# Optimization experiments

Hardware: AMD Instinct MI355X
Metric: run time of the kernel (lower is better)

## Reference

```python
import jax, jax.numpy as jnp
import numpy as np

KSIZE = 3
BJORCK_ITERS = 20
POWER_ITERS = 10


def _power_iteration_sigma(A, u):
    # A: [K, n, n], u: [K, n, 1] -> leading singular value per matrix, [K]
    for _ in range(POWER_ITERS):
        v = jnp.swapaxes(A, -1, -2) @ u
        v = v / jnp.linalg.norm(v, axis=-2, keepdims=True)
        u = A @ v
        u = u / jnp.linalg.norm(u, axis=-2, keepdims=True)
    s = (jnp.swapaxes(u, -1, -2) @ A @ v)[..., 0, 0]
    return s


def _bjorck(w, u):
    # power-iteration scaling is done under no_grad in torch -> stop_gradient
    s = jax.lax.stop_gradient(_power_iteration_sigma(jax.lax.stop_gradient(w), u))
    w = w / s[:, None, None]
    for _ in range(BJORCK_ITERS):
        wtw = jnp.swapaxes(w, -1, -2) @ w
        w = 1.5 * w - 0.5 * (w @ wtw)  # beta = 0.5, first order
    return w


def _block_orth(p1, p2):
    # -> [2, 2, n, n]
    n = p1.shape[0]
    I = jnp.eye(n, dtype=p1.dtype)
    return jnp.stack([
        jnp.stack([p1 @ p2, p1 @ (I - p2)]),
        jnp.stack([(I - p1) @ p2, (I - p1) @ (I - p2)]),
    ])


def _matrix_conv(m1, m2):
    # m1: [k,k,n,n], m2: [l,l,n,n] -> [k+l-1, k+l-1, n, n]
    k, l = m1.shape[0], m2.shape[0]
    size = k + l - 1
    rows = []
    for i in range(size):
        row = []
        for j in range(size):
            acc = 0.0
            for i1 in range(min(k, i + 1)):
                for j1 in range(min(k, j + 1)):
                    if i - i1 < l and j - j1 < l:
                        acc = acc + m1[i1, j1] @ m2[i - i1, j - j1]
            row.append(acc)
        rows.append(jnp.stack(row))
    return jnp.stack(rows)


def _bcop_weight(param_matrices, init_u):
    K, C, _ = param_matrices.shape  # K = 2*(KSIZE-1)+1, C = max_channels
    ortho = _bjorck(param_matrices, init_u)
    H = ortho[0]  # cin == cout == C, full slice
    half = C // 2
    mask = jnp.concatenate(
        [jnp.ones((K - 1, 1, half), ortho.dtype), jnp.zeros((K - 1, 1, C - half), ortho.dtype)],
        axis=-1)
    PQ = ortho[1:] * mask
    PQ = PQ @ jnp.swapaxes(PQ, -1, -2)  # symmetric projections [K-1, C, C]
    p = _block_orth(PQ[0], PQ[1])
    for t in range(1, KSIZE - 1):
        p = _matrix_conv(p, _block_orth(PQ[2 * t], PQ[2 * t + 1]))
    p = jnp.einsum('ab,ijbc->ijac', H, p)  # H @ p[i,j]
    # dict_to_tensor(...).permute(3, 2, 1, 0): [k, k, r, c] -> [c, r, j, i]
    return jnp.transpose(p, (3, 2, 1, 0))  # [C_out, C_in, KSIZE, KSIZE]


def setup_inputs() -> dict:
    key = jax.random.key(0)
    k1, k2, k3, k4 = jax.random.split(key, 4)
    C = 256
    num_kernels = 2 * (KSIZE - 1) + 1
    x = jax.random.normal(k1, (32, C, 64, 64), dtype=jnp.float32)
    param_matrices = jax.random.normal(k2, (num_kernels, C, C), dtype=jnp.float32) / np.sqrt(C)
    init_u = jax.random.normal(k3, (num_kernels, C, 1), dtype=jnp.float32)
    bias = jax.random.uniform(k4, (C,), dtype=jnp.float32, minval=-1.0 / np.sqrt(C), maxval=1.0 / np.sqrt(C))
    return {"x": x, "param_matrices": param_matrices, "init_u": init_u, "bias": bias}


def reference(x, param_matrices, init_u, bias):
    weight = _bcop_weight(param_matrices, init_u)
    # cyclic (circular) padding by k//2 on each side, odd kernel
    pad = KSIZE // 2
    xp = jnp.pad(x, ((0, 0), (0, 0), (pad, pad), (pad, pad)), mode='wrap')
    out = jax.lax.conv_general_dilated(
        xp, weight, window_strides=(1, 1), padding='VALID',
        dimension_numbers=('NCHW', 'OIHW', 'NCHW'))
    return out + bias[None, :, None, None]
```

## Files before the change

kernel.cpp:

```cpp
#include <hip/hip_runtime.h>
#include <stdint.h>

typedef unsigned short u16;
typedef unsigned short u16x4 __attribute__((ext_vector_type(4)));
typedef short bf16x8 __attribute__((ext_vector_type(8)));
typedef float f32x4 __attribute__((ext_vector_type(4)));

#define CDIM 256
#define MSZ 65536

constexpr size_t O_XB   = 0;
constexpr size_t O_AT   = 67108864;
constexpr size_t O_PQH  = 67108864;
constexpr size_t O_PQL  = O_PQH + 524288;
constexpr size_t O_SVAL = 68419584;
constexpr size_t O_W0   = 68419840;
constexpr size_t O_W1   = 71041280;
constexpr size_t O_PH   = 71041280;
constexpr size_t O_PL   = O_PH + 524288;
constexpr size_t O_QTH  = O_PL + 524288;
constexpr size_t O_QTL  = O_QTH + 524288;
constexpr size_t O_TH   = 73662720;
constexpr size_t O_TL   = O_TH + 655360;
constexpr size_t O_RTH  = 74973440;
constexpr size_t O_RTL  = O_RTH + 1179648;
constexpr size_t O_WBQ  = O_RTL + 1179648;

__device__ __forceinline__ u16 f2bf(float f) {
  union { float f; uint32_t u; } a; a.f = f;
  uint32_t u = a.u;
  uint32_t r = u + 0x7FFFu + ((u >> 16) & 1u);
  return (u16)(r >> 16);
}
__device__ __forceinline__ float bf2f(u16 u) {
  union { uint32_t u; float f; } a; a.u = ((uint32_t)u) << 16; return a.f;
}
__device__ __forceinline__ void split_st(u16* hi, u16* lo, float v) {
  u16 h = f2bf(v);
  *hi = h;
  *lo = f2bf(v - bf2f(h));
}
__device__ __forceinline__ void gl16(const void* g, void* l) {
  __builtin_amdgcn_global_load_lds(
      (const __attribute__((address_space(1))) void*)g,
      (__attribute__((address_space(3))) void*)l, 16, 0, 0);
}

__device__ __forceinline__ void cvt_block(const float* __restrict__ x,
                                          u16* __restrict__ xb, int b, char* smem) {
  float (*t)[33] = (float(*)[33])smem;
  int ctile = b & 7, wtile = (b >> 3) & 1, h = (b >> 4) & 63, n = b >> 10;
  int c0 = ctile * 32, w0 = wtile * 32;
  int tid = threadIdx.x;
  #pragma unroll
  for (int p = 0; p < 4; p++) {
    int e = tid + p * 256; int cc = e >> 5, ww = e & 31;
    t[cc][ww] = x[(((size_t)n * 256 + c0 + cc) * 64 + h) * 64 + w0 + ww];
  }
  __syncthreads();
  {
    int ww = tid >> 3, c4 = (tid & 7) * 4;
    u16x4 v;
    #pragma unroll
    for (int j = 0; j < 4; ++j) v[j] = f2bf(t[c4 + j][ww]);
    *(u16x4*)&xb[(((size_t)n * 64 + h) * 64 + w0 + ww) * 256 + c0 + c4] = v;
  }
}

__global__ void wtwA_k(const float* __restrict__ W, float* __restrict__ T) {
  int m = blockIdx.y;
  int i0 = (blockIdx.x >> 3) * 32, j0 = (blockIdx.x & 7) * 32;
  const float* A = W + (size_t)m * MSZ;
  __shared__ float As[32][33], Bs[32][33];
  int tid = threadIdx.x, tx = tid & 15, ty = tid >> 4;
  float a00 = 0, a01 = 0, a10 = 0, a11 = 0;
  for (int kc = 0; kc < CDIM; kc += 32) {
    __syncthreads();
    for (int p = 0; p < 4; p++) {
      int e = tid + p * 256; int kk = e >> 5, cc = e & 31;
      As[kk][cc] = A[(kc + kk) * CDIM + i0 + cc];
      Bs[kk][cc] = A[(kc + kk) * CDIM + j0 + cc];
    }
    __syncthreads();
    #pragma unroll
    for (int kk = 0; kk < 32; kk++) {
      float av0 = As[kk][ty], av1 = As[kk][ty + 16];
      float bv0 = Bs[kk][tx], bv1 = Bs[kk][tx + 16];
      a00 += av0 * bv0; a01 += av0 * bv1; a10 += av1 * bv0; a11 += av1 * bv1;
    }
  }
  float* Tm = T + (size_t)m * MSZ;
  Tm[(i0 + ty) * CDIM + j0 + tx] = a00;
  Tm[(i0 + ty) * CDIM + j0 + tx + 16] = a01;
  Tm[(i0 + ty + 16) * CDIM + j0 + tx] = a10;
  Tm[(i0 + ty + 16) * CDIM + j0 + tx + 16] = a11;
}

__global__ __launch_bounds__(1024) void powerB_k(const float* __restrict__ A,
                                                 const float* __restrict__ B,
                                                 const float* __restrict__ u0,
                                                 float* __restrict__ sval) {
  int m = blockIdx.x;
  int tid = threadIdx.x;
  int t = tid & 255, s = tid >> 8;
  __shared__ float v[256], part[4][257];
  const float* Am = A + (size_t)m * MSZ;
  const float* Bm = B + (size_t)m * MSZ;
  float a = 0.f;
  #pragma unroll 16
  for (int i = 0; i < 64; ++i) a += Am[(s * 64 + i) * 256 + t] * u0[m * 256 + s * 64 + i];
  part[s][t] = a;
  __syncthreads();
  if (s == 0) v[t] = part[0][t] + part[1][t] + part[2][t] + part[3][t];
  __syncthreads();
  for (int it = 0; it < 9; ++it) {
    float b = 0.f;
    #pragma unroll 16
    for (int j = 0; j < 64; ++j) b += Bm[(s * 64 + j) * 256 + t] * v[s * 64 + j];
    part[s][t] = b;
    __syncthreads();
    if (s == 0) v[t] = part[0][t] + part[1][t] + part[2][t] + part[3][t];
    __syncthreads();
  }
  float b = 0.f;
  #pragma unroll 16
  for (int j = 0; j < 64; ++j) b += Bm[(s * 64 + j) * 256 + t] * v[s * 64 + j];
  part[s][t] = b;
  __syncthreads();
  if (s == 0) {
    float w = part[0][t] + part[1][t] + part[2][t] + part[3][t];
    float vv = v[t];
    float d1 = vv * w, d2 = vv * vv;
    for (int off = 32; off; off >>= 1) {
      d1 += __shfl_down(d1, off);
      d2 += __shfl_down(d2, off);
    }
    if ((t & 63) == 0) { part[1][t >> 6] = d1; part[2][t >> 6] = d2; }
  }
  __syncthreads();
  if (tid == 0) {
    float num = part[1][0] + part[1][1] + part[1][2] + part[1][3];
    float den = part[2][0] + part[2][1] + part[2][2] + part[2][3];
    sval[m] = sqrtf(num / den);
  }
}

__global__ void scaleT_k(const float* __restrict__ param, const float* __restrict__ sval,
                         u16* __restrict__ Wh, u16* __restrict__ Wl,
                         u16* __restrict__ Wth, u16* __restrict__ Wtl) {
  __shared__ float tl[32][33];
  int m = blockIdx.y;
  int i0 = (blockIdx.x >> 3) * 32, j0 = (blockIdx.x & 7) * 32;
  int tid = threadIdx.x;
  float inv = 1.0f / sval[m];
  const float* Am = param + (size_t)m * MSZ;
  size_t mo = (size_t)m * MSZ;
  for (int p = 0; p < 4; ++p) {
    int e = tid + p * 256; int ii = e >> 5, jj = e & 31;
    float v = Am[(i0 + ii) * 256 + j0 + jj] * inv;
    tl[ii][jj] = v;
    size_t idx = mo + (size_t)(i0 + ii) * 256 + j0 + jj;
    split_st(&Wh[idx], &Wl[idx], v);
  }
  __syncthreads();
  for (int p = 0; p < 4; ++p) {
    int e = tid + p * 256; int jj = e >> 5, ii = e & 31;
    float v = tl[ii][jj];
    size_t idxT = mo + (size_t)(j0 + jj) * 256 + i0 + ii;
    split_st(&Wth[idxT], &Wtl[idxT], v);
  }
}

__device__ __forceinline__ void gemm32_acc(
    const u16* __restrict__ Ah, const u16* __restrict__ Al, int i0,
    const u16* __restrict__ Bh, const u16* __restrict__ Bl, int j0,
    int K, f32x4* acc, char* smem, int tid)
{
  int lane = tid & 63, wave = tid >> 6;
  int qm = wave >> 1, qn = wave & 1;
  int ra = qm * 16 + (lane & 15);
  int rb = qn * 16 + (lane & 15);
  int kb = (lane >> 4) * 16;
  for (int kc = 0; kc < K; kc += 128) {
    __syncthreads();
    #pragma unroll
    for (int p = 0; p < 8; ++p) {
      int e = tid + p * 256;
      int bufi = e >> 9;
      int r = (e >> 4) & 31;
      int cb = (e & 15) * 16;
      const u16* srcm = (bufi == 0) ? Ah : (bufi == 1) ? Al : (bufi == 2) ? Bh : Bl;
      int r0 = (bufi < 2) ? i0 : j0;
      const char* src = (const char*)srcm + ((size_t)(r0 + r) * 256 + kc) * 2 + cb;
      *(uint4*)(smem + bufi * 8192 + r * 256 + (cb ^ ((r & 7) << 4))) = *(const uint4*)src;
    }
    __syncthreads();
    #pragma unroll
    for (int ks = 0; ks < 4; ++ks) {
      int kbyte = ks * 64 + kb;
      int oa = ra * 256 + (kbyte ^ ((ra & 7) << 4));
      int ob = rb * 256 + (kbyte ^ ((rb & 7) << 4));
      bf16x8 ah = *(const bf16x8*)(smem + oa);
      bf16x8 al = *(const bf16x8*)(smem + 8192 + oa);
      bf16x8 bh = *(const bf16x8*)(smem + 16384 + ob);
      bf16x8 bl = *(const bf16x8*)(smem + 24576 + ob);
      *acc = __builtin_amdgcn_mfma_f32_16x16x32_bf16(ah, bh, *acc, 0, 0, 0);
      *acc = __builtin_amdgcn_mfma_f32_16x16x32_bf16(ah, bl, *acc, 0, 0, 0);
      *acc = __builtin_amdgcn_mfma_f32_16x16x32_bf16(al, bh, *acc, 0, 0, 0);
    }
  }
}

#define GEMM_IDX \
  int tid = threadIdx.x; \
  int lane = tid & 63, wave = tid >> 6, qm = wave >> 1, qn = wave & 1; \
  int orow = qm * 16 + ((lane >> 4) << 2); \
  int ocol = qn * 16 + (lane & 15); \
  int i0 = (blockIdx.x >> 3) * 32, j0 = (blockIdx.x & 7) * 32; \
  __shared__ char smem[32768];

__global__ __launch_bounds__(256) void bjorck_t_k(
    const u16* __restrict__ Wth, const u16* __restrict__ Wtl,
    u16* __restrict__ Th, u16* __restrict__ Tl,
    const float* __restrict__ x, u16* __restrict__ xb, int cvt_base) {
  __shared__ char smem[32768];
  int bx = blockIdx.x;
  if (bx >= 320) {
    int b = cvt_base + bx - 320;
    if (b < 32768) cvt_block(x, xb, b, smem);
    return;
  }
  int tid = threadIdx.x;
  int lane = tid & 63, wave = tid >> 6, qm = wave >> 1, qn = wave & 1;
  int orow = qm * 16 + ((lane >> 4) << 2);
  int ocol = qn * 16 + (lane & 15);
  int i0 = ((bx & 63) >> 3) * 32, j0 = (bx & 7) * 32;
  size_t mo = (size_t)(bx >> 6) * MSZ;
  f32x4 acc = {};
  gemm32_acc(Wth + mo, Wtl + mo, i0, Wth + mo, Wtl + mo, j0, 256, &acc, smem, tid);
  #pragma unroll
  for (int v = 0; v < 4; ++v) {
    size_t idx = mo + (size_t)(i0 + orow + v) * 256 + (j0 + ocol);
    split_st(&Th[idx], &Tl[idx], acc[v]);
  }
}

__global__ __launch_bounds__(256) void bjorck_u_k(
    const u16* __restrict__ Wh, const u16* __restrict__ Wl,
    const u16* __restrict__ Th, const u16* __restrict__ Tl,
    u16* __restrict__ nWh, u16* __restrict__ nWl,
    u16* __restrict__ nWth, u16* __restrict__ nWtl,
    const float* __restrict__ x, u16* __restrict__ xb, int cvt_base) {
  __shared__ char smem[32768];
  int bx = blockIdx.x;
  if (bx >= 320) {
    int b = cvt_base + bx - 320;
    if (b < 32768) cvt_block(x, xb, b, smem);
    return;
  }
  int tid = threadIdx.x;
  int lane = tid & 63, wave = tid >> 6, qm = wave >> 1, qn = wave & 1;
  int orow = qm * 16 + ((lane >> 4) << 2);
  int ocol = qn * 16 + (lane & 15);
  int i0 = ((bx & 63) >> 3) * 32, j0 = (bx & 7) * 32;
  size_t mo = (size_t)(bx >> 6) * MSZ;
  f32x4 acc = {};
  gemm32_acc(Wh + mo, Wl + mo, i0, Th + mo, Tl + mo, j0, 256, &acc, smem, tid);
  #pragma unroll
  for (int v = 0; v < 4; ++v) {
    int r = i0 + orow + v, c = j0 + ocol;
    size_t idx = mo + (size_t)r * 256 + c;
    float wv = bf2f(Wh[idx]) + bf2f(Wl[idx]);
    float nv = 1.5f * wv - 0.5f * acc[v];
    split_st(&nWh[idx], &nWl[idx], nv);
    size_t idxT = mo + (size_t)c * 256 + r;
    split_st(&nWth[idxT], &nWtl[idxT], nv);
  }
}

__global__ __launch_bounds__(256) void pq_k(
    const u16* __restrict__ Wh, const u16* __restrict__ Wl,
    u16* __restrict__ PQh, u16* __restrict__ PQl) {
  GEMM_IDX
  int m4 = blockIdx.y;
  const u16* Oh = Wh + (size_t)(1 + m4) * MSZ;
  const u16* Ol = Wl + (size_t)(1 + m4) * MSZ;
  f32x4 acc = {};
  gemm32_acc(Oh, Ol, i0, Oh, Ol, j0, 128, &acc, smem, tid);
  #pragma unroll
  for (int v = 0; v < 4; ++v) {
    size_t idx = (size_t)m4 * MSZ + (size_t)(i0 + orow + v) * 256 + (j0 + ocol);
    split_st(&PQh[idx], &PQl[idx], acc[v]);
  }
}

__global__ __launch_bounds__(256) void c12b_k(
    const u16* __restrict__ PQh, const u16* __restrict__ PQl,
    u16* __restrict__ Ph, u16* __restrict__ Pl,
    u16* __restrict__ QTh, u16* __restrict__ QTl) {
  GEMM_IDX
  f32x4 a1 = {}, a2t = {};
  gemm32_acc(PQh, PQl, i0, PQh + MSZ, PQl + MSZ, j0, 256, &a1, smem, tid);
  gemm32_acc(PQh + 3 * MSZ, PQl + 3 * MSZ, i0, PQh + 2 * MSZ, PQl + 2 * MSZ, j0,
             256, &a2t, smem, tid);
  #pragma unroll
  for (int v = 0; v < 4; ++v) {
    int row = i0 + orow + v, col = j0 + ocol;
    size_t g = (size_t)row * 256 + col;
    float I = (row == col) ? 1.f : 0.f;
    float p0 = bf2f(PQh[g]) + bf2f(PQl[g]);
    float p1 = bf2f(PQh[MSZ + g]) + bf2f(PQl[MSZ + g]);
    float c1 = a1[v];
    split_st(&Ph[g],           &Pl[g],           c1);
    split_st(&Ph[MSZ + g],     &Pl[MSZ + g],     p0 - c1);
    split_st(&Ph[2*MSZ + g],   &Pl[2*MSZ + g],   p1 - c1);
    split_st(&Ph[3*MSZ + g],   &Pl[3*MSZ + g],   I - p0 - p1 + c1);
    float q0 = bf2f(PQh[2*MSZ + g]) + bf2f(PQl[2*MSZ + g]);
    float q1 = bf2f(PQh[3*MSZ + g]) + bf2f(PQl[3*MSZ + g]);
    float c2t = a2t[v];
    split_st(&QTh[g],          &QTl[g],          c2t);
    split_st(&QTh[MSZ + g],    &QTl[MSZ + g],    q0 - c2t);
    split_st(&QTh[2*MSZ + g],  &QTl[2*MSZ + g],  q1 - c2t);
    split_st(&QTh[3*MSZ + g],  &QTl[3*MSZ + g],  I - q0 - q1 + c2t);
  }
}

__global__ __launch_bounds__(256) void mconv_k(
    const u16* __restrict__ Ph, const u16* __restrict__ Pl,
    const u16* __restrict__ QTh, const u16* __restrict__ QTl,
    u16* __restrict__ RTh, u16* __restrict__ RTl) {
  GEMM_IDX
  int ij = blockIdx.y;
  const int toff[10] = {0, 1, 3, 4, 6, 10, 12, 13, 15, 16};
  const int tp[16] = {0, 0, 1, 1, 0, 2, 0, 1, 2, 3, 1, 3, 2, 2, 3, 3};
  const int tq[16] = {0, 1, 0, 1, 2, 0, 3, 2, 1, 0, 3, 1, 2, 3, 2, 3};
  f32x4 acc = {};
  for (int t = toff[ij]; t < toff[ij + 1]; ++t) {
    gemm32_acc(Ph + (size_t)tp[t] * MSZ, Pl + (size_t)tp[t] * MSZ, i0,
               QTh + (size_t)tq[t] * MSZ, QTl + (size_t)tq[t] * MSZ, j0, 256, &acc, smem, tid);
  }
  #pragma unroll
  for (int v = 0; v < 4; ++v) {
    int r = i0 + orow + v, c = j0 + ocol;
    size_t idxT = (size_t)ij * MSZ + (size_t)c * 256 + r;
    split_st(&RTh[idxT], &RTl[idxT], acc[v]);
  }
}

__global__ __launch_bounds__(256) void final_k(
    const u16* __restrict__ Hh, const u16* __restrict__ Hl,
    const u16* __restrict__ RTh, const u16* __restrict__ RTl,
    u16* __restrict__ WBQ) {
  GEMM_IDX
  int ij = blockIdx.y;
  f32x4 acc = {};
  gemm32_acc(Hh, Hl, i0, RTh + (size_t)ij * MSZ, RTl + (size_t)ij * MSZ, j0,
             256, &acc, smem, tid);
  #pragma unroll
  for (int v = 0; v < 4; ++v) {
    int r = i0 + orow + v, c = j0 + ocol;
    int ct = r >> 6, ks = (r >> 5) & 1, jj = (r >> 3) & 3, e = r & 7;
    int s = jj ^ ((c >> 1) & 3);
    int g = ct * 18 + ij * 2 + ks;
    WBQ[(size_t)g * 8192 + (size_t)(c * 4 + s) * 8 + e] = f2bf(acc[v]);
  }
}

__global__ __launch_bounds__(512, 2) void conv_k(
    const u16* __restrict__ xb, const u16* __restrict__ Wb,
    const float* __restrict__ bias, float* __restrict__ out) {
  int braw = blockIdx.x;
  int L = (braw & 7) * 128 + (braw >> 3);
  int h2 = L & 31, n = L >> 5;
  int h0 = h2 * 2;
  int tid = threadIdx.x;
  int lane = tid & 63, wave = tid >> 6;
  int wm = wave >> 2, wn = wave & 3;
  int fr = lane & 15, q = lane >> 4;

  __shared__ char smem[65536];
  char* sX = smem;
  char* sW = smem + 32768;

  f32x4 acc[4][4] = {};

  auto issueX = [&](int ct) {
    #pragma unroll
    for (int i = 0; i < 4; ++i) {
      int d = (wave * 4 + i) * 64 + lane;
      int cb = (d & 7) * 16;
      int w = (d >> 3) & 63;
      int r = d >> 9;
      int hs = (h0 - 1 + r) & 63;
      const char* src = (const char*)xb + (((size_t)(n * 64 + hs) * 64 + w) << 9)
                        + ct * 128 + (cb ^ ((w & 7) << 4));
      gl16(src, sX + (wave * 4 + i) * 1024);
    }
  };
  auto issueW = [&](int g) {
    const char* base = (const char*)Wb + (size_t)g * 16384;
    char* dst = sW + (g & 1) * 16384;
    #pragma unroll
    for (int i = 0; i < 2; ++i) {
      int c = (wave * 2 + i) * 64 + lane;
      gl16(base + c * 16, dst + (wave * 2 + i) * 1024);
    }
  };

  issueX(0);
  issueW(0);
  __syncthreads();

  for (int g = 0; g < 72; ++g) {
    int ct = g / 18, r18 = g % 18, tap = r18 >> 1, ks = r18 & 1;
    int kh = tap % 3, kw = tap / 3;
    if (g + 1 < 72) issueW(g + 1);
    const char* wb = sW + (g & 1) * 16384;
    __builtin_amdgcn_s_setprio(1);
    {
      bf16x8 af[4], bfr[4];
      #pragma unroll
      for (int fn = 0; fn < 4; ++fn) {
        int cl = wn * 64 + fn * 16 + fr;
        bfr[fn] = *(const bf16x8*)(wb + cl * 64 + ((q ^ ((cl >> 1) & 3)) << 4));
      }
      int kb2 = ks * 64 + q * 16;
      #pragma unroll
      for (int fm = 0; fm < 4; ++fm) {
        int wsrc = (fm * 16 + fr + kw + 63) & 63;
        af[fm] = *(const bf16x8*)(sX + ((wm + kh) * 64 + wsrc) * 128 + (kb2 ^ ((wsrc & 7) << 4)));
      }
      #pragma unroll
      for (int fm = 0; fm < 4; ++fm)
        #pragma unroll
        for (int fn = 0; fn < 4; ++fn)
          acc[fm][fn] = __builtin_amdgcn_mfma_f32_16x16x32_bf16(af[fm], bfr[fn], acc[fm][fn], 0, 0, 0);
    }
    __builtin_amdgcn_s_setprio(0);
    if (r18 == 17 && ct < 3) {
      __syncthreads();
      issueX(ct + 1);
      __syncthreads();
    } else {
      __syncthreads();
    }
  }

  __syncthreads();
  float* sF = (float*)smem;
  #pragma unroll
  for (int r = 0; r < 2; ++r) {
    if ((wn >> 1) == r) {
      #pragma unroll
      for (int fn = 0; fn < 4; ++fn) {
        int cl = (wn & 1) * 64 + fn * 16 + fr;
        float bv = bias[r * 128 + cl];
        #pragma unroll
        for (int fm = 0; fm < 4; ++fm) {
          f32x4 v = acc[fm][fn];
          v[0] += bv; v[1] += bv; v[2] += bv; v[3] += bv;
          *(f32x4*)((char*)sF + cl * 512 + wm * 256 +
                    (((unsigned)(fm * 64 + q * 16)) ^ ((unsigned)(cl & 7) << 4))) = v;
        }
      }
    }
    __syncthreads();
    #pragma unroll
    for (int p = 0; p < 8; ++p) {
      int e = tid + p * 512;
      int w4 = e & 15, hloc = (e >> 4) & 1, cl = e >> 5;
      f32x4 val = *(const f32x4*)((const char*)sF + cl * 512 + hloc * 256 +
                                  (((unsigned)(w4 * 16)) ^ ((unsigned)(cl & 7) << 4)));
      *(f32x4*)(out + (((size_t)n * 256 + r * 128 + cl) * 64 + (h0 + hloc)) * 64 + w4 * 4) = val;
    }
    if (r == 0) __syncthreads();
  }
}

extern "C" void kernel_launch(void* const* d_in, const int* in_sizes, int n_in,
                              void* d_out, int out_size, void* d_ws, size_t ws_size,
                              hipStream_t stream) {
  const float* x = (const float*)d_in[0];
  const float* param = (const float*)d_in[1];
  const float* u0 = (const float*)d_in[2];
  const float* bias = (const float*)d_in[3];
  float* out = (float*)d_out;
  char* ws = (char*)d_ws;
  (void)in_sizes; (void)n_in; (void)out_size; (void)ws_size;

  float* B = (float*)(ws + O_AT);
  float* sval = (float*)(ws + O_SVAL);
  u16* xb = (u16*)(ws + O_XB);
  u16* W0h  = (u16*)(ws + O_W0);   u16* W0l  = W0h + 327680;
  u16* W0th = W0l + 327680;        u16* W0tl = W0th + 327680;
  u16* W1h  = (u16*)(ws + O_W1);   u16* W1l  = W1h + 327680;
  u16* W1th = W1l + 327680;        u16* W1tl = W1th + 327680;
  u16* Th = (u16*)(ws + O_TH);     u16* Tl = (u16*)(ws + O_TL);
  u16* PQh = (u16*)(ws + O_PQH);   u16* PQl = (u16*)(ws + O_PQL);
  u16* Ph = (u16*)(ws + O_PH);     u16* Pl = (u16*)(ws + O_PL);
  u16* QTh = (u16*)(ws + O_QTH);   u16* QTl = (u16*)(ws + O_QTL);
  u16* RTh = (u16*)(ws + O_RTH);   u16* RTl = (u16*)(ws + O_RTL);
  u16* WBQ = (u16*)(ws + O_WBQ);

  wtwA_k<<<dim3(64, 5), 256, 0, stream>>>(param, B);
  powerB_k<<<5, 1024, 0, stream>>>(param, B, u0, sval);
  scaleT_k<<<dim3(64, 5), 256, 0, stream>>>(param, sval, W0h, W0l, W0th, W0tl);

  u16 *cWh = W0h, *cWl = W0l, *cWth = W0th, *cWtl = W0tl;
  u16 *nWh = W1h, *nWl = W1l, *nWth = W1th, *nWtl = W1tl;
  for (int it = 0; it < 20; ++it) {
    bjorck_t_k<<<1140, 256, 0, stream>>>(cWth, cWtl, Th, Tl,
                                         x, xb, (2 * it) * 820);
    bjorck_u_k<<<1140, 256, 0, stream>>>(cWh, cWl, Th, Tl, nWh, nWl, nWth, nWtl,
                                         x, xb, (2 * it + 1) * 820);
    u16* t0;
    t0 = cWh; cWh = nWh; nWh = t0;
    t0 = cWl; cWl = nWl; nWl = t0;
    t0 = cWth; cWth = nWth; nWth = t0;
    t0 = cWtl; cWtl = nWtl; nWtl = t0;
  }

  pq_k<<<dim3(64, 4), 256, 0, stream>>>(cWh, cWl, PQh, PQl);
  c12b_k<<<64, 256, 0, stream>>>(PQh, PQl, Ph, Pl, QTh, QTl);
  mconv_k<<<dim3(64, 9), 256, 0, stream>>>(Ph, Pl, QTh, QTl, RTh, RTl);
  final_k<<<dim3(64, 9), 256, 0, stream>>>(cWh, cWl, RTh, RTl, WBQ);

  conv_k<<<1024, 512, 0, stream>>>(xb, WBQ, bias, out);
}
```

Measured before the change: 451.6 us.

## Read conv weights directly from global memory and double-buffer input tiles

The conv kernel stops staging weight slices through shared memory and has each lane load its B fragments directly from global/L2, with the weight layout rewritten to an unswizzled per-lane contiguous form. The shared memory freed this way double-buffers the input channel tiles, so the next tile's load overlaps compute. This removes the per-step barrier (now one per channel tile). In exchange, weight loads go through global memory latency inside the MFMA loop with no LDS reuse across waves.

```diff
diff --git a/kernel.cpp b/kernel.cpp
--- a/kernel.cpp
+++ b/kernel.cpp
@@ -359,10 +359,9 @@
   #pragma unroll
   for (int v = 0; v < 4; ++v) {
     int r = i0 + orow + v, c = j0 + ocol;
-    int ct = r >> 6, ks = (r >> 5) & 1, jj = (r >> 3) & 3, e = r & 7;
-    int s = jj ^ ((c >> 1) & 3);
+    int ct = r >> 6, ks = (r >> 5) & 1, qq = (r >> 3) & 3, e = r & 7;
     int g = ct * 18 + ij * 2 + ks;
-    WBQ[(size_t)g * 8192 + (size_t)(c * 4 + s) * 8 + e] = f2bf(acc[v]);
+    WBQ[(size_t)g * 8192 + (size_t)c * 32 + qq * 8 + e] = f2bf(acc[v]);
   }
 }
 
@@ -379,12 +378,10 @@
   int fr = lane & 15, q = lane >> 4;
 
   __shared__ char smem[65536];
-  char* sX = smem;
-  char* sW = smem + 32768;
 
   f32x4 acc[4][4] = {};
 
-  auto issueX = [&](int ct) {
+  auto issueX = [&](int ct, int buf) {
     #pragma unroll
     for (int i = 0; i < 4; ++i) {
       int d = (wave * 4 + i) * 64 + lane;
@@ -394,59 +391,46 @@
       int hs = (h0 - 1 + r) & 63;
       const char* src = (const char*)xb + (((size_t)(n * 64 + hs) * 64 + w) << 9)
                         + ct * 128 + (cb ^ ((w & 7) << 4));
-      gl16(src, sX + (wave * 4 + i) * 1024);
+      gl16(src, smem + buf * 32768 + (wave * 4 + i) * 1024);
     }
   };
-  auto issueW = [&](int g) {
-    const char* base = (const char*)Wb + (size_t)g * 16384;
-    char* dst = sW + (g & 1) * 16384;
-    #pragma unroll
-    for (int i = 0; i < 2; ++i) {
-      int c = (wave * 2 + i) * 64 + lane;
-      gl16(base + c * 16, dst + (wave * 2 + i) * 1024);
-    }
-  };
-
-  issueX(0);
-  issueW(0);
-  __syncthreads();
-
-  for (int g = 0; g < 72; ++g) {
-    int ct = g / 18, r18 = g % 18, tap = r18 >> 1, ks = r18 & 1;
-    int kh = tap % 3, kw = tap / 3;
-    if (g + 1 < 72) issueW(g + 1);
-    const char* wb = sW + (g & 1) * 16384;
-    __builtin_amdgcn_s_setprio(1);
-    {
-      bf16x8 af[4], bfr[4];
-      #pragma unroll
-      for (int fn = 0; fn < 4; ++fn) {
-        int cl = wn * 64 + fn * 16 + fr;
-        bfr[fn] = *(const bf16x8*)(wb + cl * 64 + ((q ^ ((cl >> 1) & 3)) << 4));
-      }
-      int kb2 = ks * 64 + q * 16;
-      #pragma unroll
-      for (int fm = 0; fm < 4; ++fm) {
-        int wsrc = (fm * 16 + fr + kw + 63) & 63;
-        af[fm] = *(const bf16x8*)(sX + ((wm + kh) * 64 + wsrc) * 128 + (kb2 ^ ((wsrc & 7) << 4)));
-      }
-      #pragma unroll
-      for (int fm = 0; fm < 4; ++fm)
+
+  issueX(0, 0);
+  __syncthreads();
+
+  const char* wlane = (const char*)Wb + (size_t)(wn * 64 + fr) * 64 + q * 16;
+
+  for (int ct = 0; ct < 4; ++ct) {
+    if (ct < 3) issueX(ct + 1, (ct + 1) & 1);
+    const char* sX = smem + (ct & 1) * 32768;
+    for (int r18 = 0; r18 < 18; ++r18) {
+      int g = ct * 18 + r18;
+      int tap = r18 >> 1, ks = r18 & 1;
+      int kh = tap % 3, kw = tap / 3;
+      __builtin_amdgcn_s_setprio(1);
+      {
+        bf16x8 af[4], bfr[4];
+        const char* wg = wlane + (size_t)g * 16384;
         #pragma unroll
         for (int fn = 0; fn < 4; ++fn)
-          acc[fm][fn] = __builtin_amdgcn_mfma_f32_16x16x32_bf16(af[fm], bfr[fn], acc[fm][fn], 0, 0, 0);
-    }
-    __builtin_amdgcn_s_setprio(0);
-    if (r18 == 17 && ct < 3) {
-      __syncthreads();
-      issueX(ct + 1);
-      __syncthreads();
-    } else {
-      __syncthreads();
-    }
-  }
-
-  __syncthreads();
+          bfr[fn] = *(const bf16x8*)(wg + fn * 1024);
+        int kb2 = ks * 64 + q * 16;
+        #pragma unroll
+        for (int fm = 0; fm < 4; ++fm) {
+          int wsrc = (fm * 16 + fr + kw + 63) & 63;
+          af[fm] = *(const bf16x8*)(sX + ((wm + kh) * 64 + wsrc) * 128 + (kb2 ^ ((wsrc & 7) << 4)));
+        }
+        #pragma unroll
+        for (int fm = 0; fm < 4; ++fm)
+          #pragma unroll
+          for (int fn = 0; fn < 4; ++fn)
+            acc[fm][fn] = __builtin_amdgcn_mfma_f32_16x16x32_bf16(af[fm], bfr[fn], acc[fm][fn], 0, 0, 0);
+      }
+      __builtin_amdgcn_s_setprio(0);
+    }
+    __syncthreads();
+  }
+
   float* sF = (float*)smem;
   #pragma unroll
   for (int r = 0; r < 2; ++r) {
```

After: 475.1 us. +5.2%, slower.
